# Performance work log

Hardware: AMD Instinct MI355X
Metric: run time of the kernel (lower is better)

The kernel has to match this reference:

```python
import jax, jax.numpy as jnp
import numpy as np

N, E = 32768, 1048576          # nodes, edges (avg degree 32)
IN, H, OUT = 128, 128, 40       # in_channels, hidden_channels, out_channels
L, R = 3, 16                    # num_layers, n_rules
EPS = 1e-5                      # BatchNorm eps


def setup_inputs() -> dict:
    key = jax.random.key(0)
    ks = jax.random.split(key, 10)
    s_in = 1.0 / np.sqrt(IN)
    s_h = 1.0 / np.sqrt(H)
    return {
        "x": jax.random.normal(ks[0], (N, IN), jnp.float32),
        "edge_index": jax.random.randint(ks[1], (2, E), 0, N, jnp.int32),
        "W_in": jax.random.normal(ks[2], (IN, H), jnp.float32) * s_in,
        "b_in": jnp.zeros((H,), jnp.float32),
        "centers": jax.random.normal(ks[3], (L, R, H), jnp.float32),
        "widths": jax.random.uniform(ks[4], (L, R, H), jnp.float32, 0.5, 1.5),
        "Wc": jax.random.normal(ks[5], (L, R, H, H), jnp.float32) * s_h,
        "bc": jnp.zeros((L, R, H), jnp.float32),
        "bn_gamma": jnp.ones((L, H), jnp.float32),
        "bn_beta": jnp.zeros((L, H), jnp.float32),
        "W_head": jax.random.normal(ks[6], (H, OUT), jnp.float32) * s_h,
        "b_head": jnp.zeros((OUT,), jnp.float32),
    }


def reference(x, edge_index, W_in, b_in, centers, widths, Wc, bc,
              bn_gamma, bn_beta, W_head, b_head):
    src, dst = edge_index[0], edge_index[1]
    n = x.shape[0]
    # in-degree for mean aggregation (clamped to 1)
    deg = jax.ops.segment_sum(jnp.ones(src.shape, x.dtype), dst, num_segments=n)
    deg = jnp.maximum(deg, 1.0)[:, None]

    h = jax.nn.relu(x @ W_in + b_in)  # [N, H]
    for l in range(L):
        # Gaussian rule memberships -> normalized firing strengths [N, R]
        d2 = (h[:, None, :] - centers[l]) ** 2 / (2.0 * widths[l] ** 2)  # [N,R,H]
        w = jax.nn.softmax(-jnp.mean(d2, axis=-1), axis=-1)              # [N,R]
        # TSK rule consequents (per-rule linear) and firing-weighted mix
        y = jnp.einsum('nh,rho->nro', h, Wc[l]) + bc[l]                  # [N,R,H]
        msg = jnp.einsum('nr,nro->no', w, y)                             # [N,H]
        # edge gather (src) + scatter-mean to dst
        agg = jax.ops.segment_sum(msg[src], dst, num_segments=n) / deg   # [N,H]
        # relu -> BatchNorm1d (batch statistics) -> residual (dropout=eval)
        a = jax.nn.relu(agg)
        mu = jnp.mean(a, axis=0)
        var = jnp.var(a, axis=0)
        a = (a - mu) * jax.lax.rsqrt(var + EPS) * bn_gamma[l] + bn_beta[l]
        h = h + a
    return jax.nn.softmax(h @ W_head + b_head, axis=-1)  # [N, OUT]
```

## Files before the change

### kernel.cpp

```cpp
#include <hip/hip_runtime.h>
#include <hip/hip_bf16.h>
#include <stdint.h>


#define NN 32768
#define NE 1048576
#define H 128
#define R 16
#define NL 3
#define ODIM 40
#define NB 4096

typedef short bf16x8 __attribute__((ext_vector_type(8)));
typedef float f32x4 __attribute__((ext_vector_type(4)));
typedef unsigned short u16x4 __attribute__((ext_vector_type(4)));

__device__ inline short f2bf_rne(float f) {
    unsigned u = __float_as_uint(f);
    u += 0x7FFFu + ((u >> 16) & 1u);
    return (short)(u >> 16);
}
__device__ inline void split_bf(float v, short& hi, short& lo) {
    unsigned u = __float_as_uint(v);
    unsigned uh = (u + 0x7FFFu + ((u >> 16) & 1u)) & 0xFFFF0000u;
    hi = (short)(uh >> 16);
    lo = f2bf_rne(v - __uint_as_float(uh));
}
__device__ inline f32x4 bf4f(u16x4 v) {
    f32x4 r;
    r.x = __uint_as_float((unsigned)v.x << 16);
    r.y = __uint_as_float((unsigned)v.y << 16);
    r.z = __uint_as_float((unsigned)v.z << 16);
    r.w = __uint_as_float((unsigned)v.w << 16);
    return r;
}
__device__ inline void gload_lds16(const void* g, void* l) {
    __builtin_amdgcn_global_load_lds(
        (const __attribute__((address_space(1))) unsigned*)g,
        (__attribute__((address_space(3))) unsigned*)l, 16, 0, 0);
}

__device__ inline f32x4 bn4(f32x4 hv, f32x4 av, f32x4 s1, f32x4 s2, f32x4 gm,
                            f32x4 bt) {
    f32x4 r;
#define BN_C(X)                                               \
    {                                                         \
        float mu = s1.X * (1.0f / NN);                        \
        float var = s2.X * (1.0f / NN) - mu * mu;             \
        float inv = rsqrtf(var + 1e-5f);                      \
        r.X = hv.X + (av.X - mu) * inv * gm.X + bt.X;         \
    }
    BN_C(x) BN_C(y) BN_C(z) BN_C(w)
#undef BN_C
    return r;
}

__global__ __launch_bounds__(256) void k_prep_all(
    const float* __restrict__ Wc, short* __restrict__ WcT,
    const float* __restrict__ W_in, short* __restrict__ WinHi,
    short* __restrict__ WinLo, const float* __restrict__ W_head,
    short* __restrict__ WhHi, short* __restrict__ WhLo,
    const float* __restrict__ widths, float* __restrict__ IW,
    int* __restrict__ bcnt) {
    int bid = blockIdx.x, tid = threadIdx.x;
    if (bid < 3072) {
        int s = bid * 256 + tid;
        int lr = s >> 14;
        int rem = s & 16383;
        int k = rem >> 7, o = rem & 127;
        int kb = k >> 3;
        int d = lr * 16384 + o * 128 + (((kb ^ (o & 7)) << 3)) + (k & 7);
        WcT[d] = f2bf_rne(Wc[s]);
    } else if (bid < 3136) {
        int t = (bid - 3072) * 256 + tid;
        int k = t >> 7, o = t & 127;
        int kb = k >> 3;
        int d = o * 128 + (((kb ^ (o & 7)) << 3)) + (k & 7);
        short hi, lo;
        split_bf(W_in[k * 128 + o], hi, lo);
        WinHi[d] = hi;
        WinLo[d] = lo;
    } else if (bid < 3160) {
        int t = (bid - 3136) * 256 + tid;
        int o = t >> 7, k = t & 127;
        float v = (o < ODIM) ? W_head[k * ODIM + o] : 0.0f;
        int kb = k >> 3;
        int d = o * 128 + (((kb ^ (o & 7)) << 3)) + (k & 7);
        short hi, lo;
        split_bf(v, hi, lo);
        WhHi[d] = hi;
        WhLo[d] = lo;
    } else if (bid < 3184) {
        int t = (bid - 3160) * 256 + tid;
        float wd = widths[t];
        IW[t] = 0.5f / (wd * wd) * (1.0f / 128.0f);
    } else {
        int i = (bid - 3184) * 256 + tid;
        if (i < NB) bcnt[i] = 0;
    }
}

__global__ __launch_bounds__(1024) void k_histb(const int* __restrict__ dst,
                                                int* __restrict__ bcnt) {
    __shared__ int hist[NB];
    for (int i = threadIdx.x; i < NB; i += 1024) hist[i] = 0;
    __syncthreads();
    int base = blockIdx.x * 8192;
    for (int i = threadIdx.x; i < 8192; i += 1024)
        atomicAdd(&hist[dst[base + i] >> 3], 1);
    __syncthreads();
    for (int i = threadIdx.x; i < NB; i += 1024) {
        int c = hist[i];
        if (c) atomicAdd(&bcnt[i], c);
    }
}

__global__ __launch_bounds__(1024) void k_scanb(const int* __restrict__ bcnt,
                                                int* __restrict__ bstart,
                                                int* __restrict__ cursor,
                                                float* __restrict__ sumsAll) {
    __shared__ int ssum[1024];
    int t = threadIdx.x;
    if (t < 768) sumsAll[t] = 0.0f;
    int c0 = bcnt[t * 4], c1 = bcnt[t * 4 + 1];
    int c2 = bcnt[t * 4 + 2], c3 = bcnt[t * 4 + 3];
    ssum[t] = c0 + c1 + c2 + c3;
    __syncthreads();
    for (int off = 1; off < 1024; off <<= 1) {
        int v = (t >= off) ? ssum[t - off] : 0;
        __syncthreads();
        ssum[t] += v;
        __syncthreads();
    }
    int run = (t == 0) ? 0 : ssum[t - 1];
    bstart[t * 4] = run; cursor[t * 4] = run; run += c0;
    bstart[t * 4 + 1] = run; cursor[t * 4 + 1] = run; run += c1;
    bstart[t * 4 + 2] = run; cursor[t * 4 + 2] = run; run += c2;
    bstart[t * 4 + 3] = run; cursor[t * 4 + 3] = run; run += c3;
    if (t == 1023) bstart[NB] = run;
}

__global__ void k_fillb(const int* __restrict__ src, const int* __restrict__ dst,
                        int* __restrict__ cursor, int* __restrict__ ebuf) {
    int e = blockIdx.x * 256 + threadIdx.x;
    int d = dst[e], s = src[e];
    int p = atomicAdd(&cursor[d >> 3], 1);
    ebuf[p] = s | ((d & 7) << 15);
}

__global__ __launch_bounds__(64) void k_sortb(const int* __restrict__ bstart,
                                              const int* __restrict__ ebuf,
                                              int* __restrict__ esrc,
                                              int* __restrict__ row_start) {
    __shared__ int cnt[8], cur[8];
    int b = blockIdx.x, lane = threadIdx.x;
    int st = bstart[b], en = bstart[b + 1];
    if (lane < 8) cnt[lane] = 0;
    __syncthreads();
    for (int i = st + lane; i < en; i += 64)
        atomicAdd(&cnt[(ebuf[i] >> 15) & 7], 1);
    __syncthreads();
    if (lane == 0) {
        int run = st;
#pragma unroll
        for (int k = 0; k < 8; k++) {
            row_start[b * 8 + k] = run;
            cur[k] = run;
            run += cnt[k];
        }
        if (b == NB - 1) row_start[NN] = run;
    }
    __syncthreads();
    for (int i = st + lane; i < en; i += 64) {
        int e = ebuf[i];
        int p = atomicAdd(&cur[(e >> 15) & 7], 1);
        esrc[p] = e & 32767;
    }
}

__global__ __launch_bounds__(256, 2) void k_in_mfma(
    const float* __restrict__ x, const short* __restrict__ Whi,
    const short* __restrict__ Wlo, const float* __restrict__ b,
    float* __restrict__ h) {
    __shared__ short Bs[16384];
    int tid = threadIdx.x, lane = tid & 63, wv = tid >> 6;
    int quad = lane >> 4, lm = lane & 15;
    int row0 = blockIdx.x * 64;
    int m = row0 + wv * 16 + lm;

    bf16x8 ahi[4], alo[4];
#pragma unroll
    for (int kc = 0; kc < 4; kc++) {
        f32x4 va = *(const f32x4*)(x + m * H + kc * 32 + quad * 8);
        f32x4 vb = *(const f32x4*)(x + m * H + kc * 32 + quad * 8 + 4);
        float vv[8] = {va.x, va.y, va.z, va.w, vb.x, vb.y, vb.z, vb.w};
#pragma unroll
        for (int j = 0; j < 8; j++) {
            short hi, lo;
            split_bf(vv[j], hi, lo);
            ahi[kc][j] = hi;
            alo[kc][j] = lo;
        }
    }
    f32x4 acc[8];
#pragma unroll
    for (int c = 0; c < 8; c++) acc[c] = (f32x4){0.f, 0.f, 0.f, 0.f};

    char* ldst = (char*)Bs + wv * 8192;
    const char* g1 = (const char*)Whi + wv * 8192 + lane * 16;
#pragma unroll
    for (int cc = 0; cc < 8; cc++) gload_lds16(g1 + cc * 1024, ldst + cc * 1024);
    __syncthreads();
#pragma unroll
    for (int kc = 0; kc < 4; kc++)
#pragma unroll
        for (int c = 0; c < 8; c++) {
            int o = c * 16 + lm;
            bf16x8 bfr = *(const bf16x8*)&Bs[o * 128 + (((kc * 4 + quad) ^ (o & 7)) << 3)];
            acc[c] = __builtin_amdgcn_mfma_f32_16x16x32_bf16(ahi[kc], bfr, acc[c], 0, 0, 0);
            acc[c] = __builtin_amdgcn_mfma_f32_16x16x32_bf16(alo[kc], bfr, acc[c], 0, 0, 0);
        }
    __syncthreads();
    const char* g2 = (const char*)Wlo + wv * 8192 + lane * 16;
#pragma unroll
    for (int cc = 0; cc < 8; cc++) gload_lds16(g2 + cc * 1024, ldst + cc * 1024);
    __syncthreads();
#pragma unroll
    for (int kc = 0; kc < 4; kc++)
#pragma unroll
        for (int c = 0; c < 8; c++) {
            int o = c * 16 + lm;
            bf16x8 bfr = *(const bf16x8*)&Bs[o * 128 + (((kc * 4 + quad) ^ (o & 7)) << 3)];
            acc[c] = __builtin_amdgcn_mfma_f32_16x16x32_bf16(ahi[kc], bfr, acc[c], 0, 0, 0);
        }
    int orow = row0 + wv * 16 + quad * 4;
#pragma unroll
    for (int c = 0; c < 8; c++) {
        int col = c * 16 + lm;
        float bi = b[col];
#pragma unroll
        for (int v = 0; v < 4; v++)
            h[(orow + v) * H + col] = fmaxf(acc[c][v] + bi, 0.0f);
    }
}

__global__ __launch_bounds__(256, 2) void k_gemm3(
    const float* __restrict__ h, const float* __restrict__ aprev,
    const float* __restrict__ sums, const float* __restrict__ gamma,
    const float* __restrict__ beta, const short* __restrict__ BT,
    const float* __restrict__ bc, const float* __restrict__ cen,
    const float* __restrict__ iw, unsigned short* __restrict__ msgb,
    float* __restrict__ hout) {
    __shared__ __align__(16) char smemu[33792];
    short* Bs = (short*)smemu;
    float(*hs)[132] = (float(*)[132])smemu;
    __shared__ float wsh[16][64];
    __shared__ float sm[64][17];

    int tid = threadIdx.x, lane = tid & 63, wv = tid >> 6;
    int quad = lane >> 4, lm = lane & 15;
    int row0 = blockIdx.x * 64;

    if (gamma) {
        for (int g = tid; g < 2048; g += 256) {
            int rr = g >> 5, cc = (g & 31) << 2;
            int grow = row0 + rr;
            f32x4 hv = *(const f32x4*)&h[grow * H + cc];
            f32x4 av = *(const f32x4*)&aprev[grow * H + cc];
            f32x4 r = bn4(hv, av, *(const f32x4*)&sums[cc],
                          *(const f32x4*)&sums[H + cc],
                          *(const f32x4*)&gamma[cc], *(const f32x4*)&beta[cc]);
            *(f32x4*)&hs[rr][cc] = r;
            *(f32x4*)&hout[grow * H + cc] = r;
        }
    } else {
        const f32x4* hg = (const f32x4*)(h + row0 * H);
        for (int g = tid; g < 2048; g += 256) {
            int rr = g >> 5, cc = (g & 31) << 2;
            *(f32x4*)&hs[rr][cc] = hg[g];
        }
    }
    __syncthreads();

    {
        int wvu = __builtin_amdgcn_readfirstlane(wv);
        const float* c0 = cen + (wvu * 4 + 0) * H;
        const float* c1 = cen + (wvu * 4 + 1) * H;
        const float* c2 = cen + (wvu * 4 + 2) * H;
        const float* c3 = cen + (wvu * 4 + 3) * H;
        const float* w0 = iw + (wvu * 4 + 0) * H;
        const float* w1 = iw + (wvu * 4 + 1) * H;
        const float* w2 = iw + (wvu * 4 + 2) * H;
        const float* w3 = iw + (wvu * 4 + 3) * H;
        float s0 = 0.f, s1 = 0.f, s2 = 0.f, s3 = 0.f;
#pragma unroll 4
        for (int j0 = 0; j0 < H; j0 += 4) {
            f32x4 hv = *(const f32x4*)&hs[lane][j0];
            f32x4 cv, wv4, d;
            cv = *(const f32x4*)(c0 + j0); wv4 = *(const f32x4*)(w0 + j0);
            d = hv - cv;
            s0 += d.x * d.x * wv4.x + d.y * d.y * wv4.y + d.z * d.z * wv4.z + d.w * d.w * wv4.w;
            cv = *(const f32x4*)(c1 + j0); wv4 = *(const f32x4*)(w1 + j0);
            d = hv - cv;
            s1 += d.x * d.x * wv4.x + d.y * d.y * wv4.y + d.z * d.z * wv4.z + d.w * d.w * wv4.w;
            cv = *(const f32x4*)(c2 + j0); wv4 = *(const f32x4*)(w2 + j0);
            d = hv - cv;
            s2 += d.x * d.x * wv4.x + d.y * d.y * wv4.y + d.z * d.z * wv4.z + d.w * d.w * wv4.w;
            cv = *(const f32x4*)(c3 + j0); wv4 = *(const f32x4*)(w3 + j0);
            d = hv - cv;
            s3 += d.x * d.x * wv4.x + d.y * d.y * wv4.y + d.z * d.z * wv4.z + d.w * d.w * wv4.w;
        }
        sm[lane][wvu * 4 + 0] = s0;
        sm[lane][wvu * 4 + 1] = s1;
        sm[lane][wvu * 4 + 2] = s2;
        sm[lane][wvu * 4 + 3] = s3;
    }

    bf16x8 ahi[4], alo[4];
    {
        int m = wv * 16 + lm;
#pragma unroll
        for (int kc = 0; kc < 4; kc++) {
            f32x4 va = *(const f32x4*)&hs[m][kc * 32 + quad * 8];
            f32x4 vb = *(const f32x4*)&hs[m][kc * 32 + quad * 8 + 4];
            float vv[8] = {va.x, va.y, va.z, va.w, vb.x, vb.y, vb.z, vb.w};
#pragma unroll
            for (int j = 0; j < 8; j++) {
                short hi, lo;
                split_bf(vv[j], hi, lo);
                ahi[kc][j] = hi;
                alo[kc][j] = lo;
            }
        }
    }
    __syncthreads();

    if (tid < 64) {
        float v[16], mx = -1e30f;
#pragma unroll
        for (int r = 0; r < R; r++) {
            v[r] = -sm[tid][r];
            mx = fmaxf(mx, v[r]);
        }
        float sum = 0.f, e[16];
#pragma unroll
        for (int r = 0; r < R; r++) {
            e[r] = __expf(v[r] - mx);
            sum += e[r];
        }
        float inv = 1.0f / sum;
#pragma unroll
        for (int r = 0; r < R; r++) wsh[r][tid] = e[r] * inv;
    }

    f32x4 out[8];
#pragma unroll
    for (int c = 0; c < 8; c++) out[c] = (f32x4){0.f, 0.f, 0.f, 0.f};

    char* ldst = (char*)Bs + wv * 8192;
    for (int r = 0; r < R; r++) {
        __syncthreads();
        const char* gsrc = (const char*)(BT + r * 16384) + wv * 8192 + lane * 16;
#pragma unroll
        for (int cc = 0; cc < 8; cc++) gload_lds16(gsrc + cc * 1024, ldst + cc * 1024);
        __syncthreads();

        f32x4 accr[8];
#pragma unroll
        for (int c = 0; c < 8; c++) accr[c] = (f32x4){0.f, 0.f, 0.f, 0.f};
#pragma unroll
        for (int kc = 0; kc < 4; kc++)
#pragma unroll
            for (int c = 0; c < 8; c++) {
                int o = c * 16 + lm;
                bf16x8 bfr = *(const bf16x8*)&Bs[o * 128 + (((kc * 4 + quad) ^ (o & 7)) << 3)];
                accr[c] = __builtin_amdgcn_mfma_f32_16x16x32_bf16(ahi[kc], bfr, accr[c], 0, 0, 0);
                accr[c] = __builtin_amdgcn_mfma_f32_16x16x32_bf16(alo[kc], bfr, accr[c], 0, 0, 0);
            }
        f32x4 wr4 = *(const f32x4*)&wsh[r][wv * 16 + quad * 4];
#pragma unroll
        for (int c = 0; c < 8; c++) {
            out[c].x += wr4.x * accr[c].x;
            out[c].y += wr4.y * accr[c].y;
            out[c].z += wr4.z * accr[c].z;
            out[c].w += wr4.w * accr[c].w;
        }
    }

    __syncthreads();
    for (int g = tid; g < 512; g += 256) {
        int o = g >> 2, kb = g & 3;
        bf16x8 v;
#pragma unroll
        for (int j = 0; j < 8; j++) {
            int k = kb * 8 + j;
            v[j] = (k < R) ? f2bf_rne(bc[k * H + o]) : (short)0;
        }
        *(bf16x8*)&Bs[o * 128 + ((kb ^ (o & 7)) << 3)] = v;
    }
    bf16x8 abias;
#pragma unroll
    for (int j = 0; j < 8; j++)
        abias[j] = (quad < 2) ? f2bf_rne(wsh[quad * 8 + j][wv * 16 + lm]) : (short)0;
    __syncthreads();
#pragma unroll
    for (int c = 0; c < 8; c++) {
        int o = c * 16 + lm;
        bf16x8 bfr = *(const bf16x8*)&Bs[o * 128 + ((quad ^ (o & 7)) << 3)];
        out[c] = __builtin_amdgcn_mfma_f32_16x16x32_bf16(abias, bfr, out[c], 0, 0, 0);
    }

    int orow = row0 + wv * 16 + quad * 4;
#pragma unroll
    for (int c = 0; c < 8; c++) {
        int col = c * 16 + lm;
#pragma unroll
        for (int v = 0; v < 4; v++)
            msgb[(orow + v) * H + col] = (unsigned short)f2bf_rne(out[c][v]);
    }
}

__global__ __launch_bounds__(256) void k_agg(
    const unsigned short* __restrict__ msgb, const int* __restrict__ row_start,
    const int* __restrict__ esrc, float* __restrict__ a) {
    int tid = threadIdx.x;
    int g = tid >> 5, lane = tid & 31;
    int n = blockIdx.x * 8 + g;
    int b = row_start[n], e = row_start[n + 1];
    f32x4 a0 = {0.f, 0.f, 0.f, 0.f}, a1 = a0, a2 = a0, a3 = a0;
    int i = b;
    for (; i + 4 <= e; i += 4) {
        int s0 = esrc[i], s1 = esrc[i + 1], s2 = esrc[i + 2], s3 = esrc[i + 3];
        a0 += bf4f(*(const u16x4*)&msgb[s0 * H + lane * 4]);
        a1 += bf4f(*(const u16x4*)&msgb[s1 * H + lane * 4]);
        a2 += bf4f(*(const u16x4*)&msgb[s2 * H + lane * 4]);
        a3 += bf4f(*(const u16x4*)&msgb[s3 * H + lane * 4]);
    }
    for (; i < e; i++)
        a0 += bf4f(*(const u16x4*)&msgb[esrc[i] * H + lane * 4]);
    f32x4 t = (a0 + a1) + (a2 + a3);
    float id = 1.0f / fmaxf((float)(e - b), 1.0f);
    f32x4 res;
    res.x = fmaxf(t.x * id, 0.f);
    res.y = fmaxf(t.y * id, 0.f);
    res.z = fmaxf(t.z * id, 0.f);
    res.w = fmaxf(t.w * id, 0.f);
    *(f32x4*)&a[n * H + lane * 4] = res;
}

__global__ __launch_bounds__(128) void k_bnstats(const float* __restrict__ a,
                                                 float* __restrict__ sums) {
    int t = threadIdx.x;
    float s = 0.0f, s2 = 0.0f;
    for (int n = blockIdx.x; n < NN; n += gridDim.x) {
        float v = a[n * H + t];
        s += v;
        s2 += v * v;
    }
    atomicAdd(&sums[t], s);
    atomicAdd(&sums[H + t], s2);
}

__global__ __launch_bounds__(256, 2) void k_head2(
    const float* __restrict__ h, const float* __restrict__ aprev,
    const float* __restrict__ sums, const float* __restrict__ gamma,
    const float* __restrict__ beta, const short* __restrict__ Whi,
    const short* __restrict__ Wlo, const float* __restrict__ bh,
    float* __restrict__ out) {
    __shared__ short Bs[12288];
    int tid = threadIdx.x, lane = tid & 63, wv = tid >> 6;
    int quad = lane >> 4, lm = lane & 15;
    int row0 = blockIdx.x * 64;
    int m = row0 + wv * 16 + lm;

    bf16x8 ahi[4], alo[4];
#pragma unroll
    for (int kc = 0; kc < 4; kc++) {
        int base = kc * 32 + quad * 8;
        f32x4 hv0 = *(const f32x4*)&h[m * H + base];
        f32x4 hv1 = *(const f32x4*)&h[m * H + base + 4];
        f32x4 av0 = *(const f32x4*)&aprev[m * H + base];
        f32x4 av1 = *(const f32x4*)&aprev[m * H + base + 4];
        f32x4 r0 = bn4(hv0, av0, *(const f32x4*)&sums[base],
                       *(const f32x4*)&sums[H + base],
                       *(const f32x4*)&gamma[base], *(const f32x4*)&beta[base]);
        f32x4 r1 = bn4(hv1, av1, *(const f32x4*)&sums[base + 4],
                       *(const f32x4*)&sums[H + base + 4],
                       *(const f32x4*)&gamma[base + 4],
                       *(const f32x4*)&beta[base + 4]);
        float vv[8] = {r0.x, r0.y, r0.z, r0.w, r1.x, r1.y, r1.z, r1.w};
#pragma unroll
        for (int j = 0; j < 8; j++) {
            short hi, lo;
            split_bf(vv[j], hi, lo);
            ahi[kc][j] = hi;
            alo[kc][j] = lo;
        }
    }
    {
        char* ldst = (char*)Bs + wv * 3072;
        const char* g1 = (const char*)Whi + wv * 3072 + lane * 16;
        const char* g2 = (const char*)Wlo + wv * 3072 + lane * 16;
#pragma unroll
        for (int cc = 0; cc < 3; cc++) gload_lds16(g1 + cc * 1024, ldst + cc * 1024);
        char* ldst2 = (char*)Bs + 12288 + wv * 3072;
#pragma unroll
        for (int cc = 0; cc < 3; cc++) gload_lds16(g2 + cc * 1024, ldst2 + cc * 1024);
    }
    __syncthreads();
    f32x4 acc[3];
#pragma unroll
    for (int c = 0; c < 3; c++) acc[c] = (f32x4){0.f, 0.f, 0.f, 0.f};
#pragma unroll
    for (int kc = 0; kc < 4; kc++)
#pragma unroll
        for (int c = 0; c < 3; c++) {
            int o = c * 16 + lm;
            int off = o * 128 + (((kc * 4 + quad) ^ (o & 7)) << 3);
            bf16x8 bH = *(const bf16x8*)&Bs[off];
            bf16x8 bL = *(const bf16x8*)&Bs[6144 + off];
            acc[c] = __builtin_amdgcn_mfma_f32_16x16x32_bf16(ahi[kc], bH, acc[c], 0, 0, 0);
            acc[c] = __builtin_amdgcn_mfma_f32_16x16x32_bf16(alo[kc], bH, acc[c], 0, 0, 0);
            acc[c] = __builtin_amdgcn_mfma_f32_16x16x32_bf16(ahi[kc], bL, acc[c], 0, 0, 0);
        }
    float bh0 = bh[lm], bh1 = bh[16 + lm];
    float bh2 = (lm < 8) ? bh[32 + lm] : 0.f;
    int orow = row0 + wv * 16 + quad * 4;
#pragma unroll
    for (int v = 0; v < 4; v++) {
        float v0 = acc[0][v] + bh0;
        float v1 = acc[1][v] + bh1;
        float v2 = (lm < 8) ? (acc[2][v] + bh2) : -1e30f;
        float mx = fmaxf(fmaxf(v0, v1), v2);
        for (int off = 8; off; off >>= 1) mx = fmaxf(mx, __shfl_xor(mx, off, 16));
        float e0 = __expf(v0 - mx), e1 = __expf(v1 - mx);
        float e2 = (lm < 8) ? __expf(v2 - mx) : 0.f;
        float s = e0 + e1 + e2;
        for (int off = 8; off; off >>= 1) s += __shfl_xor(s, off, 16);
        float inv = 1.0f / s;
        out[(orow + v) * ODIM + lm] = e0 * inv;
        out[(orow + v) * ODIM + 16 + lm] = e1 * inv;
        if (lm < 8) out[(orow + v) * ODIM + 32 + lm] = e2 * inv;
    }
}

extern "C" void kernel_launch(void* const* d_in, const int* in_sizes, int n_in,
                              void* d_out, int out_size, void* d_ws, size_t ws_size,
                              hipStream_t stream) {
    const float* x = (const float*)d_in[0];
    const int* edge_index = (const int*)d_in[1];
    const float* W_in = (const float*)d_in[2];
    const float* b_in = (const float*)d_in[3];
    const float* centers = (const float*)d_in[4];
    const float* widths = (const float*)d_in[5];
    const float* Wc = (const float*)d_in[6];
    const float* bc = (const float*)d_in[7];
    const float* bn_gamma = (const float*)d_in[8];
    const float* bn_beta = (const float*)d_in[9];
    const float* W_head = (const float*)d_in[10];
    const float* b_head = (const float*)d_in[11];
    float* out = (float*)d_out;

    const int* src = edge_index;
    const int* dst = edge_index + NE;

    float* h = (float*)d_ws;
    float* a = h + NN * H;
    float* sumsAll = a + NN * H;
    float* IW = sumsAll + 768;
    int* bcnt = (int*)(IW + NL * R * H);
    int* cursor = bcnt + NB;
    int* bstart = cursor + NB;
    int* row_start = bstart + NB + 1;
    int* ebuf = row_start + NN + 1;
    int* esrc = ebuf + NE;
    uintptr_t p = (uintptr_t)(esrc + NE);
    p = (p + 63) & ~(uintptr_t)63;
    unsigned short* msgb = (unsigned short*)p;
    short* WcT = (short*)(msgb + NN * H);
    short* WinHi = WcT + NL * R * H * H;
    short* WinLo = WinHi + 16384;
    short* WhHi = WinLo + 16384;
    short* WhLo = WhHi + 6144;

    k_prep_all<<<3200, 256, 0, stream>>>(Wc, WcT, W_in, WinHi, WinLo, W_head,
                                         WhHi, WhLo, widths, IW, bcnt);
    k_histb<<<128, 1024, 0, stream>>>(dst, bcnt);
    k_scanb<<<1, 1024, 0, stream>>>(bcnt, bstart, cursor, sumsAll);
    k_fillb<<<NE / 256, 256, 0, stream>>>(src, dst, cursor, ebuf);
    k_sortb<<<NB, 64, 0, stream>>>(bstart, ebuf, esrc, row_start);

    k_in_mfma<<<NN / 64, 256, 0, stream>>>(x, WinHi, WinLo, b_in, h);

    for (int l = 0; l < NL; l++) {
        const float* gm = (l == 0) ? nullptr : bn_gamma + (l - 1) * H;
        const float* bt = (l == 0) ? nullptr : bn_beta + (l - 1) * H;
        const float* sm = (l == 0) ? nullptr : sumsAll + 256 * (l - 1);
        k_gemm3<<<NN / 64, 256, 0, stream>>>(h, a, sm, gm, bt,
                                             WcT + l * R * H * H, bc + l * R * H,
                                             centers + l * R * H, IW + l * R * H,
                                             msgb, h);
        k_agg<<<NN / 8, 256, 0, stream>>>(msgb, row_start, esrc, a);
        k_bnstats<<<512, 128, 0, stream>>>(a, sumsAll + 256 * l);
    }
    k_head2<<<NN / 64, 256, 0, stream>>>(h, a, sumsAll + 512, bn_gamma + 2 * H,
                                         bn_beta + 2 * H, WhHi, WhLo, b_head, out);
}
```

Baseline: 549.6 us.

## Replace fine-grained bucket CSR build with 64-bin partition and per-bin sort

```diff
diff --git a/kernel.cpp b/kernel.cpp
--- a/kernel.cpp
+++ b/kernel.cpp
@@ -9,7 +9,8 @@
 #define R 16
 #define NL 3
 #define ODIM 40
-#define NB 4096
+#define NBIN 64
+#define BINCAP 18432
 
 typedef short bf16x8 __attribute__((ext_vector_type(8)));
 typedef float f32x4 __attribute__((ext_vector_type(4)));
@@ -61,7 +62,7 @@
     short* __restrict__ WinLo, const float* __restrict__ W_head,
     short* __restrict__ WhHi, short* __restrict__ WhLo,
     const float* __restrict__ widths, float* __restrict__ IW,
-    int* __restrict__ bcnt) {
+    int* __restrict__ binCnt) {
     int bid = blockIdx.x, tid = threadIdx.x;
     if (bid < 3072) {
         int s = bid * 256 + tid;
@@ -95,86 +96,82 @@
         float wd = widths[t];
         IW[t] = 0.5f / (wd * wd) * (1.0f / 128.0f);
     } else {
-        int i = (bid - 3184) * 256 + tid;
-        if (i < NB) bcnt[i] = 0;
-    }
-}
-
-__global__ __launch_bounds__(1024) void k_histb(const int* __restrict__ dst,
-                                                int* __restrict__ bcnt) {
-    __shared__ int hist[NB];
-    for (int i = threadIdx.x; i < NB; i += 1024) hist[i] = 0;
-    __syncthreads();
-    int base = blockIdx.x * 8192;
-    for (int i = threadIdx.x; i < 8192; i += 1024)
-        atomicAdd(&hist[dst[base + i] >> 3], 1);
-    __syncthreads();
-    for (int i = threadIdx.x; i < NB; i += 1024) {
-        int c = hist[i];
-        if (c) atomicAdd(&bcnt[i], c);
-    }
-}
-
-__global__ __launch_bounds__(1024) void k_scanb(const int* __restrict__ bcnt,
-                                                int* __restrict__ bstart,
-                                                int* __restrict__ cursor,
-                                                float* __restrict__ sumsAll) {
-    __shared__ int ssum[1024];
+        if (tid < NBIN) binCnt[tid] = 0;
+    }
+}
+
+__global__ __launch_bounds__(256) void k_part(const int* __restrict__ src,
+                                              const int* __restrict__ dst,
+                                              int* __restrict__ binCnt,
+                                              int* __restrict__ pbuf) {
+    __shared__ int hist[NBIN];
+    int tid = threadIdx.x;
+    int e0 = blockIdx.x * 8192;
+    if (tid < NBIN) hist[tid] = 0;
+    __syncthreads();
+    for (int i = tid; i < 8192; i += 256)
+        atomicAdd(&hist[dst[e0 + i] >> 9], 1);
+    __syncthreads();
+    if (tid < NBIN) hist[tid] = atomicAdd(&binCnt[tid], hist[tid]);
+    __syncthreads();
+    for (int i = tid; i < 8192; i += 256) {
+        int d = dst[e0 + i], s = src[e0 + i];
+        int b = d >> 9;
+        int p = atomicAdd(&hist[b], 1);
+        pbuf[b * BINCAP + p] = s | ((d & 511) << 15);
+    }
+}
+
+__global__ __launch_bounds__(64) void k_scan64(const int* __restrict__ binCnt,
+                                               int* __restrict__ binStart,
+                                               int* __restrict__ row_start,
+                                               float* __restrict__ sumsAll) {
     int t = threadIdx.x;
-    if (t < 768) sumsAll[t] = 0.0f;
-    int c0 = bcnt[t * 4], c1 = bcnt[t * 4 + 1];
-    int c2 = bcnt[t * 4 + 2], c3 = bcnt[t * 4 + 3];
-    ssum[t] = c0 + c1 + c2 + c3;
-    __syncthreads();
-    for (int off = 1; off < 1024; off <<= 1) {
-        int v = (t >= off) ? ssum[t - off] : 0;
+    for (int i = t; i < 768; i += 64) sumsAll[i] = 0.0f;
+    int c = binCnt[t];
+    int v = c;
+    for (int off = 1; off < 64; off <<= 1) {
+        int u = __shfl_up(v, off);
+        if (t >= off) v += u;
+    }
+    binStart[t] = v - c;
+    if (t == 63) {
+        binStart[NBIN] = v;
+        row_start[NN] = v;
+    }
+}
+
+__global__ __launch_bounds__(512) void k_sortp(const int* __restrict__ binCnt,
+                                               const int* __restrict__ binStart,
+                                               const int* __restrict__ pbuf,
+                                               int* __restrict__ esrc,
+                                               int* __restrict__ row_start) {
+    __shared__ int cnt[512], sc[512], cur[512];
+    int b = blockIdx.x, t = threadIdx.x;
+    int n = binCnt[b];
+    int gbase = binStart[b];
+    const int* p = pbuf + b * BINCAP;
+    cnt[t] = 0;
+    __syncthreads();
+    for (int i = t; i < n; i += 512)
+        atomicAdd(&cnt[(p[i] >> 15) & 511], 1);
+    __syncthreads();
+    sc[t] = cnt[t];
+    __syncthreads();
+    for (int off = 1; off < 512; off <<= 1) {
+        int v = (t >= off) ? sc[t - off] : 0;
         __syncthreads();
-        ssum[t] += v;
+        sc[t] += v;
         __syncthreads();
     }
-    int run = (t == 0) ? 0 : ssum[t - 1];
-    bstart[t * 4] = run; cursor[t * 4] = run; run += c0;
-    bstart[t * 4 + 1] = run; cursor[t * 4 + 1] = run; run += c1;
-    bstart[t * 4 + 2] = run; cursor[t * 4 + 2] = run; run += c2;
-    bstart[t * 4 + 3] = run; cursor[t * 4 + 3] = run; run += c3;
-    if (t == 1023) bstart[NB] = run;
-}
-
-__global__ void k_fillb(const int* __restrict__ src, const int* __restrict__ dst,
-                        int* __restrict__ cursor, int* __restrict__ ebuf) {
-    int e = blockIdx.x * 256 + threadIdx.x;
-    int d = dst[e], s = src[e];
-    int p = atomicAdd(&cursor[d >> 3], 1);
-    ebuf[p] = s | ((d & 7) << 15);
-}
-
-__global__ __launch_bounds__(64) void k_sortb(const int* __restrict__ bstart,
-                                              const int* __restrict__ ebuf,
-                                              int* __restrict__ esrc,
-                                              int* __restrict__ row_start) {
-    __shared__ int cnt[8], cur[8];
-    int b = blockIdx.x, lane = threadIdx.x;
-    int st = bstart[b], en = bstart[b + 1];
-    if (lane < 8) cnt[lane] = 0;
-    __syncthreads();
-    for (int i = st + lane; i < en; i += 64)
-        atomicAdd(&cnt[(ebuf[i] >> 15) & 7], 1);
-    __syncthreads();
-    if (lane == 0) {
-        int run = st;
-#pragma unroll
-        for (int k = 0; k < 8; k++) {
-            row_start[b * 8 + k] = run;
-            cur[k] = run;
-            run += cnt[k];
-        }
-        if (b == NB - 1) row_start[NN] = run;
-    }
-    __syncthreads();
-    for (int i = st + lane; i < en; i += 64) {
-        int e = ebuf[i];
-        int p = atomicAdd(&cur[(e >> 15) & 7], 1);
-        esrc[p] = e & 32767;
+    int start = gbase + sc[t] - cnt[t];
+    row_start[b * 512 + t] = start;
+    cur[t] = start;
+    __syncthreads();
+    for (int i = t; i < n; i += 512) {
+        int e = p[i];
+        int pos = atomicAdd(&cur[(e >> 15) & 511], 1);
+        esrc[pos] = e & 32767;
     }
 }
 
@@ -428,17 +425,23 @@
     int n = blockIdx.x * 8 + g;
     int b = row_start[n], e = row_start[n + 1];
     f32x4 a0 = {0.f, 0.f, 0.f, 0.f}, a1 = a0, a2 = a0, a3 = a0;
+    f32x4 a4 = a0, a5 = a0, a6 = a0, a7 = a0;
     int i = b;
-    for (; i + 4 <= e; i += 4) {
+    for (; i + 8 <= e; i += 8) {
         int s0 = esrc[i], s1 = esrc[i + 1], s2 = esrc[i + 2], s3 = esrc[i + 3];
+        int s4 = esrc[i + 4], s5 = esrc[i + 5], s6 = esrc[i + 6], s7 = esrc[i + 7];
         a0 += bf4f(*(const u16x4*)&msgb[s0 * H + lane * 4]);
         a1 += bf4f(*(const u16x4*)&msgb[s1 * H + lane * 4]);
         a2 += bf4f(*(const u16x4*)&msgb[s2 * H + lane * 4]);
         a3 += bf4f(*(const u16x4*)&msgb[s3 * H + lane * 4]);
+        a4 += bf4f(*(const u16x4*)&msgb[s4 * H + lane * 4]);
+        a5 += bf4f(*(const u16x4*)&msgb[s5 * H + lane * 4]);
+        a6 += bf4f(*(const u16x4*)&msgb[s6 * H + lane * 4]);
+        a7 += bf4f(*(const u16x4*)&msgb[s7 * H + lane * 4]);
     }
     for (; i < e; i++)
         a0 += bf4f(*(const u16x4*)&msgb[esrc[i] * H + lane * 4]);
-    f32x4 t = (a0 + a1) + (a2 + a3);
+    f32x4 t = ((a0 + a1) + (a2 + a3)) + ((a4 + a5) + (a6 + a7));
     float id = 1.0f / fmaxf((float)(e - b), 1.0f);
     f32x4 res;
     res.x = fmaxf(t.x * id, 0.f);
@@ -568,12 +571,11 @@
     float* a = h + NN * H;
     float* sumsAll = a + NN * H;
     float* IW = sumsAll + 768;
-    int* bcnt = (int*)(IW + NL * R * H);
-    int* cursor = bcnt + NB;
-    int* bstart = cursor + NB;
-    int* row_start = bstart + NB + 1;
-    int* ebuf = row_start + NN + 1;
-    int* esrc = ebuf + NE;
+    int* binCnt = (int*)(IW + NL * R * H);
+    int* binStart = binCnt + NBIN;
+    int* row_start = binStart + NBIN + 1;
+    int* pbuf = row_start + NN + 1;
+    int* esrc = pbuf + NBIN * BINCAP;
     uintptr_t p = (uintptr_t)(esrc + NE);
     p = (p + 63) & ~(uintptr_t)63;
     unsigned short* msgb = (unsigned short*)p;
@@ -583,12 +585,11 @@
     short* WhHi = WinLo + 16384;
     short* WhLo = WhHi + 6144;
 
-    k_prep_all<<<3200, 256, 0, stream>>>(Wc, WcT, W_in, WinHi, WinLo, W_head,
-                                         WhHi, WhLo, widths, IW, bcnt);
-    k_histb<<<128, 1024, 0, stream>>>(dst, bcnt);
-    k_scanb<<<1, 1024, 0, stream>>>(bcnt, bstart, cursor, sumsAll);
-    k_fillb<<<NE / 256, 256, 0, stream>>>(src, dst, cursor, ebuf);
-    k_sortb<<<NB, 64, 0, stream>>>(bstart, ebuf, esrc, row_start);
+    k_prep_all<<<3185, 256, 0, stream>>>(Wc, WcT, W_in, WinHi, WinLo, W_head,
+                                         WhHi, WhLo, widths, IW, binCnt);
+    k_part<<<NE / 8192, 256, 0, stream>>>(src, dst, binCnt, pbuf);
+    k_scan64<<<1, 64, 0, stream>>>(binCnt, binStart, row_start, sumsAll);
+    k_sortp<<<NBIN, 512, 0, stream>>>(binCnt, binStart, pbuf, esrc, row_start);
 
     k_in_mfma<<<NN / 64, 256, 0, stream>>>(x, WinHi, WinLo, b_in, h);
 
```

After: 509.8 us. 1.08x faster.
